# Kernel optimization log

Hardware: AMD Instinct MI355X
Metric: run time of the kernel (lower is better)

The kernel has to match this reference:

```python
import jax, jax.numpy as jnp
import numpy as np

B, S, H = 1, 2048, 2048
NH, NKV, HD = 16, 4, 128          # heads, kv heads, head_dim
RHD = 64                          # rope head dim
QC, KVC = 1536, 512               # q / kv latent dims
EPS = 1e-6
SCALE = (HD + RHD) ** -0.5


def rms_norm(x, w):
    var = jnp.mean(x.astype(jnp.float32) ** 2, axis=-1, keepdims=True)
    return (x * jax.lax.rsqrt(var + EPS) * w).astype(x.dtype)


def rotate_half(x):
    x1, x2 = x[..., : x.shape[-1] // 2], x[..., x.shape[-1] // 2:]
    return jnp.concatenate([-x2, x1], axis=-1)


def apply_rope(q, k, cos, sin):
    cos = cos[:, None, :, :]  # [B,1,S,RHD]
    sin = sin[:, None, :, :]
    return q * cos + rotate_half(q) * sin, k * cos + rotate_half(k) * sin


def setup_inputs() -> dict:
    key = jax.random.key(0)
    ks = jax.random.split(key, 12)
    X = jax.random.normal(ks[0], (B, S, H), jnp.float32)
    # rotary tables
    inv_freq = 1.0 / (10000.0 ** (np.arange(0, RHD, 2, dtype=np.float32) / RHD))
    t = np.arange(S, dtype=np.float32)
    freqs = np.outer(t, inv_freq)               # [S, RHD/2]
    emb = np.concatenate([freqs, freqs], -1)    # [S, RHD]
    cos = jnp.asarray(np.cos(emb))[None].repeat(B, 0)
    sin = jnp.asarray(np.sin(emb))[None].repeat(B, 0)
    mask = jnp.tril(jnp.ones((S, S), jnp.int32))[None].repeat(B, 0)  # causal
    sc = lambda fan_in: 1.0 / np.sqrt(fan_in)
    return dict(
        X=X, cos=cos, sin=sin, mask=mask,
        w_down_q=jax.random.normal(ks[1], (H, QC), jnp.float32) * sc(H),
        w_up_q=jax.random.normal(ks[2], (QC, H), jnp.float32) * sc(QC),
        w_qr=jax.random.normal(ks[3], (QC, NH * RHD), jnp.float32) * sc(QC),
        w_down_kv=jax.random.normal(ks[4], (H, KVC), jnp.float32) * sc(H),
        w_up_k=jax.random.normal(ks[5], (KVC, NKV * HD), jnp.float32) * sc(KVC),
        w_up_v=jax.random.normal(ks[6], (KVC, NKV * HD), jnp.float32) * sc(KVC),
        w_kr=jax.random.normal(ks[7], (H, RHD), jnp.float32) * sc(H),
        w_o=jax.random.normal(ks[8], (H, H), jnp.float32) * sc(H),
        q_norm_w=jnp.ones((QC,), jnp.float32),
        k_norm_w=jnp.ones((KVC,), jnp.float32),
    )


def reference(X, cos, sin, mask, w_down_q, w_up_q, w_qr, w_down_kv,
              w_up_k, w_up_v, w_kr, w_o, q_norm_w, k_norm_w):
    bsz, q_len, _ = X.shape
    n_rep = NH // NKV
    # --- Q path: down-project, RMSNorm, up-project + rope branch ---
    cq = rms_norm(X @ w_down_q, q_norm_w)                    # [B,S,QC]
    qc = (cq @ w_up_q).reshape(bsz, q_len, NH, HD).transpose(0, 2, 1, 3)
    qr = (cq @ w_qr).reshape(bsz, q_len, NH, RHD).transpose(0, 2, 1, 3)
    # --- KV path ---
    ckv = rms_norm(X @ w_down_kv, k_norm_w)                  # [B,S,KVC]
    kc = (ckv @ w_up_k).reshape(bsz, q_len, NKV, HD).transpose(0, 2, 1, 3)
    kr = (X @ w_kr).reshape(bsz, q_len, 1, RHD).transpose(0, 2, 1, 3)
    kc = jnp.repeat(kc, n_rep, axis=1)                       # [B,NH,S,HD]
    kr = jnp.broadcast_to(kr, (bsz, NH, q_len, RHD))         # repeat_kv(kr, NH)
    qr, kr = apply_rope(qr, kr, cos, sin)
    query = jnp.concatenate([qc, qr], axis=-1)               # [B,NH,S,HD+RHD]
    key = jnp.concatenate([kc, kr], axis=-1)
    value = (ckv @ w_up_v).reshape(bsz, q_len, NKV, HD).transpose(0, 2, 1, 3)
    value = jnp.repeat(value, n_rep, axis=1)                 # [B,NH,S,HD]
    # --- attention ---
    scores = jnp.einsum('bhqd,bhkd->bhqk', query, key) * SCALE
    scores = jnp.where(mask[:, None] == 0, -1e9, scores)
    attn = jax.nn.softmax(scores, axis=-1)                   # dropout p=0
    ctx = jnp.einsum('bhqk,bhkd->bhqd', attn, value)
    ctx = ctx.transpose(0, 2, 1, 3).reshape(bsz, q_len, NH * HD)
    return ctx @ w_o, attn
```

## Files before the change

### kernel.cpp

```cpp
#include <hip/hip_runtime.h>
#include <stdint.h>

typedef __bf16 bf16;
typedef __bf16 bf16x8 __attribute__((ext_vector_type(8)));
typedef __bf16 bf16x4 __attribute__((ext_vector_type(4)));
typedef float f32x4 __attribute__((ext_vector_type(4)));

#define DEVFN static __device__ __forceinline__

constexpr int S = 2048, Hdim = 2048, NH = 16, NKV = 4, HD = 128, RHD = 64, QC = 1536, KVC = 512;
constexpr int QKD = HD + RHD;
constexpr int DN = 2112;
constexpr float RMS_EPS = 1e-6f;
constexpr float ATT_SCALE = 0.07216878364870323f;

DEVFN float wave_sum(float v) {
#pragma unroll
  for (int o = 32; o > 0; o >>= 1) v += __shfl_xor(v, o, 64);
  return v;
}
DEVFN float block_sum(float v) {
  __shared__ float red_s[4];
  v = wave_sum(v);
  int lane = threadIdx.x & 63, wid = threadIdx.x >> 6;
  if (lane == 0) red_s[wid] = v;
  __syncthreads();
  v = red_s[0] + red_s[1] + red_s[2] + red_s[3];
  __syncthreads();
  return v;
}

DEVFN void lgkm_barrier() {
  asm volatile("s_waitcnt lgkmcnt(0)" ::: "memory");
  __builtin_amdgcn_s_barrier();
}

DEVFN void gload16(const bf16* g, bf16* l) {
  __builtin_amdgcn_global_load_lds(
      (const __attribute__((address_space(1))) uint32_t*)g,
      (__attribute__((address_space(3))) uint32_t*)l, 16, 0, 0);
}

template <typename OT>
DEVFN void gemm_core_async(const bf16* __restrict__ A, const bf16* __restrict__ Bt,
                           OT* __restrict__ C, int N, int lda, int ldb, int ldc,
                           int m0, int n0, float scale, int kend) {
  __shared__ alignas(16) bf16 As[128 * 32];
  __shared__ alignas(16) bf16 Bs[128 * 32];
  const int t = threadIdx.x;
  const int lane = t & 63;
  const int wm = ((t >> 7) & 1) * 64;
  const int wn = ((t >> 6) & 1) * 64;
  const int lr = lane & 15;
  const int lk = (lane >> 4) * 8;
  const int srow = t >> 2;
  const int scol = (t & 3) * 8;
  const bf16* Ab = A + (size_t)(m0 + srow) * lda + scol;
  const bf16* Bb = Bt + (size_t)(n0 + srow) * ldb + scol;
  bf16* Al = As + t * 8;
  bf16* Bl = Bs + t * 8;

  f32x4 acc[4][4];
#pragma unroll
  for (int i = 0; i < 4; i++)
#pragma unroll
    for (int j = 0; j < 4; j++) { f32x4 z = {0.f, 0.f, 0.f, 0.f}; acc[i][j] = z; }

  for (int kk = 0; kk < kend; kk += 32) {
    gload16(Ab + kk, Al);
    gload16(Ab + (size_t)64 * lda + kk, Al + 2048);
    gload16(Bb + kk, Bl);
    gload16(Bb + (size_t)64 * ldb + kk, Bl + 2048);
    __syncthreads();
    bf16x8 a[4], b[4];
#pragma unroll
    for (int i = 0; i < 4; i++)
      a[i] = *reinterpret_cast<const bf16x8*>(&As[(wm + i * 16 + lr) * 32 + lk]);
#pragma unroll
    for (int i = 0; i < 4; i++)
      b[i] = *reinterpret_cast<const bf16x8*>(&Bs[(wn + i * 16 + lr) * 32 + lk]);
#pragma unroll
    for (int i = 0; i < 4; i++)
#pragma unroll
      for (int j = 0; j < 4; j++)
        acc[i][j] = __builtin_amdgcn_mfma_f32_16x16x32_bf16(a[i], b[j], acc[i][j], 0, 0, 0);
    __syncthreads();
  }
  const int orow = (lane >> 4) * 4;
#pragma unroll
  for (int i = 0; i < 4; i++) {
#pragma unroll
    for (int j = 0; j < 4; j++) {
      int col = n0 + wn + j * 16 + lr;
      if (col < N) {
#pragma unroll
        for (int q = 0; q < 4; q++) {
          int row = m0 + wm + i * 16 + orow + q;
          C[(size_t)row * ldc + col] = (OT)(acc[i][j][q] * scale);
        }
      }
    }
  }
}

template <typename OT>
__global__ __launch_bounds__(256) void gemm_nt(const bf16* __restrict__ A, const bf16* __restrict__ Bt,
                                               OT* __restrict__ C, int N, int K, int lda,
                                               int ldb, int ldc, float scale) {
  gemm_core_async<OT>(A, Bt, C, N, lda, ldb, ldc, blockIdx.y * 128, blockIdx.x * 128, scale, K);
}

__global__ __launch_bounds__(256) void gemm_up_both(const bf16* __restrict__ cqb,
                                                    const bf16* __restrict__ ckvb,
                                                    const bf16* __restrict__ wt_up1,
                                                    const bf16* __restrict__ wt_up2,
                                                    bf16* __restrict__ up1,
                                                    bf16* __restrict__ up2) {
  int id = blockIdx.x;
  if (id < 384) {
    gemm_core_async<bf16>(cqb, wt_up1, up1, 3072, QC, QC, 3072, (id / 24) * 128, (id % 24) * 128, 1.f, QC);
  } else {
    id -= 384;
    gemm_core_async<bf16>(ckvb, wt_up2, up2, 1024, KVC, KVC, 1024, (id / 8) * 128, (id % 8) * 128, 1.f, KVC);
  }
}

__global__ __launch_bounds__(512) void fa_fused(const bf16* __restrict__ qpack,
                                                const bf16* __restrict__ kpack,
                                                const bf16* __restrict__ vt,
                                                float* __restrict__ attn,
                                                bf16* __restrict__ ctxb) {
  const int h = blockIdx.y;
  const int g = h >> 2;
  __shared__ alignas(16) bf16 Qs[64 * 200];
  __shared__ alignas(16) bf16 Ks[2][64 * 200];
  __shared__ alignas(16) bf16 Ps[64 * 72];
  __shared__ alignas(16) bf16 Vs[2][128 * 72];
  float2* sb = reinterpret_cast<float2*>(Ps);
  float2* statf = sb + 128;

  const int t = threadIdx.x;
  const int lane = t & 63;
  const int w = t >> 6;
  const int wm = (w & 3) * 16;
  const int kh = w >> 2;
  const int lr = lane & 15;
  const int hi = lane >> 4;
  const int lk = hi * 8;
  const int kr0 = t / 24, kc0 = (t % 24) * 8;
  const int kr1 = (t + 512) / 24, kc1 = ((t + 512) % 24) * 8;
  const int kr2 = (t + 1024) / 24, kc2 = ((t + 1024) % 24) * 8;
  const int vr0 = t >> 3, vc0 = (t & 7) * 8;
  const int vr1 = (t + 512) >> 3, vc1 = ((t + 512) & 7) * 8;

  const bf16* Qg = qpack + (size_t)h * S * QKD;
  const bf16* Kg = kpack + (size_t)g * S * QKD;
  const bf16* Vg = vt + (size_t)g * HD * S;
  float* Ah = attn + (size_t)h * S * S;
  bf16* C = ctxb + h * HD;

  for (int sub = 0; sub < 2; ++sub) {
    const int m0 = sub ? (1984 - 64 * blockIdx.x) : (64 * blockIdx.x);
    const int ntiles = sub ? (32 - blockIdx.x) : (blockIdx.x + 1);
    const int kend = m0 + 64;
    __syncthreads();
    *reinterpret_cast<bf16x8*>(&Qs[kr0 * 200 + kc0]) =
        *reinterpret_cast<const bf16x8*>(&Qg[(size_t)(m0 + kr0) * QKD + kc0]);
    *reinterpret_cast<bf16x8*>(&Qs[kr1 * 200 + kc1]) =
        *reinterpret_cast<const bf16x8*>(&Qg[(size_t)(m0 + kr1) * QKD + kc1]);
    *reinterpret_cast<bf16x8*>(&Qs[kr2 * 200 + kc2]) =
        *reinterpret_cast<const bf16x8*>(&Qg[(size_t)(m0 + kr2) * QKD + kc2]);

    float mreg[4] = {-1e30f, -1e30f, -1e30f, -1e30f};
    float lreg[4] = {0.f, 0.f, 0.f, 0.f};
    bf16x8 ck0 = *reinterpret_cast<const bf16x8*>(&Kg[(size_t)kr0 * QKD + kc0]);
    bf16x8 ck1 = *reinterpret_cast<const bf16x8*>(&Kg[(size_t)kr1 * QKD + kc1]);
    bf16x8 ck2 = *reinterpret_cast<const bf16x8*>(&Kg[(size_t)kr2 * QKD + kc2]);
    int cur = 0;
    for (int ti = 0; ti < ntiles; ++ti) {
      const int kt = ti * 64;
      bf16x8 nk0, nk1, nk2;
      if (ti + 1 < ntiles) {
        nk0 = *reinterpret_cast<const bf16x8*>(&Kg[(size_t)(kt + 64 + kr0) * QKD + kc0]);
        nk1 = *reinterpret_cast<const bf16x8*>(&Kg[(size_t)(kt + 64 + kr1) * QKD + kc1]);
        nk2 = *reinterpret_cast<const bf16x8*>(&Kg[(size_t)(kt + 64 + kr2) * QKD + kc2]);
      }
      *reinterpret_cast<bf16x8*>(&Ks[cur][kr0 * 200 + kc0]) = ck0;
      *reinterpret_cast<bf16x8*>(&Ks[cur][kr1 * 200 + kc1]) = ck1;
      *reinterpret_cast<bf16x8*>(&Ks[cur][kr2 * 200 + kc2]) = ck2;
      lgkm_barrier();
      f32x4 acc[2];
#pragma unroll
      for (int kb = 0; kb < 2; kb++) { f32x4 z = {0.f, 0.f, 0.f, 0.f}; acc[kb] = z; }
#pragma unroll
      for (int ks = 0; ks < 6; ++ks) {
        bf16x8 a = *reinterpret_cast<const bf16x8*>(&Qs[(wm + lr) * 200 + ks * 32 + lk]);
#pragma unroll
        for (int kb = 0; kb < 2; ++kb) {
          bf16x8 b = *reinterpret_cast<const bf16x8*>(&Ks[cur][(kh * 32 + kb * 16 + lr) * 200 + ks * 32 + lk]);
          acc[kb] = __builtin_amdgcn_mfma_f32_16x16x32_bf16(a, b, acc[kb], 0, 0, 0);
        }
      }
      const int colb = kt + kh * 32 + lr;
#pragma unroll
      for (int q = 0; q < 4; ++q) {
        const int rowg = m0 + wm + hi * 4 + q;
        bool u0 = (colb <= rowg), u1 = (colb + 16 <= rowg);
        float s0 = u0 ? acc[0][q] * ATT_SCALE : -1e30f;
        float s1 = u1 ? acc[1][q] * ATT_SCALE : -1e30f;
        float nm = fmaxf(mreg[q], fmaxf(s0, s1));
        float e0 = u0 ? __expf(s0 - nm) : 0.f;
        float e1 = u1 ? __expf(s1 - nm) : 0.f;
        lreg[q] = lreg[q] * __expf(mreg[q] - nm) + e0 + e1;
        mreg[q] = nm;
      }
      ck0 = nk0; ck1 = nk1; ck2 = nk2;
      cur ^= 1;
    }
#pragma unroll
    for (int q = 0; q < 4; ++q) {
      float m = mreg[q], l = lreg[q];
#pragma unroll
      for (int o = 1; o < 16; o <<= 1) {
        float mo = __shfl_xor(m, o, 64);
        float lo = __shfl_xor(l, o, 64);
        float M = fmaxf(m, mo);
        l = l * __expf(m - M) + lo * __expf(mo - M);
        m = M;
      }
      mreg[q] = m; lreg[q] = l;
    }
    __syncthreads();
    if (lr == 0) {
#pragma unroll
      for (int q = 0; q < 4; ++q)
        sb[kh * 64 + wm + hi * 4 + q] = make_float2(mreg[q], lreg[q]);
    }
    __syncthreads();
    if (w < 4 && lr == 0) {
#pragma unroll
      for (int q = 0; q < 4; ++q) {
        int r = wm + hi * 4 + q;
        float2 a = sb[r], b = sb[64 + r];
        float M = fmaxf(a.x, b.x);
        float L = a.y * __expf(a.x - M) + b.y * __expf(b.x - M);
        statf[r] = make_float2(M, 1.0f / L);
      }
    }
    __syncthreads();
    float mr[4], invl[4];
#pragma unroll
    for (int q = 0; q < 4; ++q) {
      float2 sv = statf[wm + hi * 4 + q];
      mr[q] = sv.x; invl[q] = sv.y;
    }
    __syncthreads();

    f32x4 accp[4];
#pragma unroll
    for (int j = 0; j < 4; j++) { f32x4 z = {0.f, 0.f, 0.f, 0.f}; accp[j] = z; }
    ck0 = *reinterpret_cast<const bf16x8*>(&Kg[(size_t)kr0 * QKD + kc0]);
    ck1 = *reinterpret_cast<const bf16x8*>(&Kg[(size_t)kr1 * QKD + kc1]);
    ck2 = *reinterpret_cast<const bf16x8*>(&Kg[(size_t)kr2 * QKD + kc2]);
    bf16x8 cv0 = *reinterpret_cast<const bf16x8*>(&Vg[(size_t)vr0 * S + vc0]);
    bf16x8 cv1 = *reinterpret_cast<const bf16x8*>(&Vg[(size_t)vr1 * S + vc1]);
    cur = 0;
    for (int ti = 0; ti < ntiles; ++ti) {
      const int kt = ti * 64;
      bf16x8 nk0, nk1, nk2, nv0, nv1;
      if (ti + 1 < ntiles) {
        nk0 = *reinterpret_cast<const bf16x8*>(&Kg[(size_t)(kt + 64 + kr0) * QKD + kc0]);
        nk1 = *reinterpret_cast<const bf16x8*>(&Kg[(size_t)(kt + 64 + kr1) * QKD + kc1]);
        nk2 = *reinterpret_cast<const bf16x8*>(&Kg[(size_t)(kt + 64 + kr2) * QKD + kc2]);
        nv0 = *reinterpret_cast<const bf16x8*>(&Vg[(size_t)vr0 * S + kt + 64 + vc0]);
        nv1 = *reinterpret_cast<const bf16x8*>(&Vg[(size_t)vr1 * S + kt + 64 + vc1]);
      }
      *reinterpret_cast<bf16x8*>(&Ks[cur][kr0 * 200 + kc0]) = ck0;
      *reinterpret_cast<bf16x8*>(&Ks[cur][kr1 * 200 + kc1]) = ck1;
      *reinterpret_cast<bf16x8*>(&Ks[cur][kr2 * 200 + kc2]) = ck2;
      *reinterpret_cast<bf16x8*>(&Vs[cur][vr0 * 72 + vc0]) = cv0;
      *reinterpret_cast<bf16x8*>(&Vs[cur][vr1 * 72 + vc1]) = cv1;
      lgkm_barrier();
      f32x4 acc[2];
#pragma unroll
      for (int kb = 0; kb < 2; kb++) { f32x4 z = {0.f, 0.f, 0.f, 0.f}; acc[kb] = z; }
#pragma unroll
      for (int ks = 0; ks < 6; ++ks) {
        bf16x8 a = *reinterpret_cast<const bf16x8*>(&Qs[(wm + lr) * 200 + ks * 32 + lk]);
#pragma unroll
        for (int kb = 0; kb < 2; ++kb) {
          bf16x8 b = *reinterpret_cast<const bf16x8*>(&Ks[cur][(kh * 32 + kb * 16 + lr) * 200 + ks * 32 + lk]);
          acc[kb] = __builtin_amdgcn_mfma_f32_16x16x32_bf16(a, b, acc[kb], 0, 0, 0);
        }
      }
      const int colb = kt + kh * 32 + lr;
#pragma unroll
      for (int kb = 0; kb < 2; ++kb) {
#pragma unroll
        for (int q = 0; q < 4; ++q) {
          const int rloc = wm + hi * 4 + q;
          const int rowg = m0 + rloc;
          const int col = colb + kb * 16;
          float s = acc[kb][q] * ATT_SCALE;
          float p = (col <= rowg) ? __expf(s - mr[q]) * invl[q] : 0.f;
          Ah[(size_t)rowg * S + col] = p;
          Ps[rloc * 72 + kh * 32 + kb * 16 + lr] = (bf16)p;
        }
      }
      lgkm_barrier();
#pragma unroll
      for (int ks = 0; ks < 2; ++ks) {
        bf16x8 a = *reinterpret_cast<const bf16x8*>(&Ps[(wm + lr) * 72 + ks * 32 + lk]);
#pragma unroll
        for (int j = 0; j < 4; ++j) {
          bf16x8 b = *reinterpret_cast<const bf16x8*>(&Vs[cur][(kh * 64 + j * 16 + lr) * 72 + ks * 32 + lk]);
          accp[j] = __builtin_amdgcn_mfma_f32_16x16x32_bf16(a, b, accp[j], 0, 0, 0);
        }
      }
      ck0 = nk0; ck1 = nk1; ck2 = nk2; cv0 = nv0; cv1 = nv1;
      cur ^= 1;
    }

    const float4 zz = make_float4(0.f, 0.f, 0.f, 0.f);
    {
      const int zr = t >> 3, zc0 = (t & 7) * 4;
      float* zrow = Ah + (size_t)(m0 + zr) * S;
      for (int k = kend + zc0; k < S; k += 32) *reinterpret_cast<float4*>(zrow + k) = zz;
    }

#pragma unroll
    for (int j = 0; j < 4; ++j) {
      const int d = kh * 64 + j * 16 + lr;
#pragma unroll
      for (int q = 0; q < 4; ++q) {
        const int rowg = m0 + wm + hi * 4 + q;
        C[(size_t)rowg * Hdim + d] = (bf16)accp[j][q];
      }
    }
  }
}

struct TJobs {
  const float* src[8];
  bf16* dst[8];
  int R[8], C[8], tiles[8];
};

__global__ __launch_bounds__(256) void prep(const float* __restrict__ Xf,
                                            bf16* __restrict__ Xb, TJobs J) {
  const int t = threadIdx.x;
  int id = blockIdx.x;
  if (id < 2048) {
    size_t i = (size_t)id * 256 + t;
    float4 f0 = *reinterpret_cast<const float4*>(Xf + i * 8);
    float4 f1 = *reinterpret_cast<const float4*>(Xf + i * 8 + 4);
    bf16x8 v;
    v[0] = (bf16)f0.x; v[1] = (bf16)f0.y; v[2] = (bf16)f0.z; v[3] = (bf16)f0.w;
    v[4] = (bf16)f1.x; v[5] = (bf16)f1.y; v[6] = (bf16)f1.z; v[7] = (bf16)f1.w;
    *reinterpret_cast<bf16x8*>(Xb + i * 8) = v;
    return;
  }
  int tile = id - 2048;
  int j = 0;
  while (tile >= J.tiles[j]) { tile -= J.tiles[j]; ++j; }
  const int C = J.C[j], R = J.R[j];
  int tcn = C >> 5;
  int rb = (tile / tcn) * 32, cb = (tile % tcn) * 32;
  const float* in = J.src[j];
  bf16* out = J.dst[j];
  __shared__ float tl[32][33];
  int tx = t & 31, ty = t >> 5;
#pragma unroll
  for (int q = 0; q < 32; q += 8)
    tl[ty + q][tx] = in[(size_t)(rb + ty + q) * C + cb + tx];
  __syncthreads();
#pragma unroll
  for (int q = 0; q < 32; q += 8)
    out[(size_t)(cb + ty + q) * R + rb + tx] = (bf16)tl[tx][ty + q];
}

__global__ __launch_bounds__(256) void rmsnorm_fused(const float* __restrict__ dproj,
                                                     const float* __restrict__ qw,
                                                     const float* __restrict__ kw,
                                                     bf16* __restrict__ cqb,
                                                     bf16* __restrict__ ckvb) {
  int row = blockIdx.x;
  bool isq = (blockIdx.y == 0);
  int C = isq ? QC : KVC;
  const float* p = dproj + (size_t)row * DN + (isq ? 0 : QC);
  const float* w = isq ? qw : kw;
  bf16* out = (isq ? cqb : ckvb) + (size_t)row * C;
  float ss = 0.f;
  for (int i = threadIdx.x * 4; i < C; i += 1024) {
    float4 v = *reinterpret_cast<const float4*>(p + i);
    ss += v.x * v.x + v.y * v.y + v.z * v.z + v.w * v.w;
  }
  ss = block_sum(ss);
  float r = rsqrtf(ss / (float)C + RMS_EPS);
  for (int i = threadIdx.x * 4; i < C; i += 1024) {
    float4 v = *reinterpret_cast<const float4*>(p + i);
    float4 g = *reinterpret_cast<const float4*>(w + i);
    bf16x4 o;
    o[0] = (bf16)(v.x * r * g.x); o[1] = (bf16)(v.y * r * g.y);
    o[2] = (bf16)(v.z * r * g.z); o[3] = (bf16)(v.w * r * g.w);
    *reinterpret_cast<bf16x4*>(out + i) = o;
  }
}

__global__ __launch_bounds__(256) void pack_all(const bf16* __restrict__ up1,
                                                const bf16* __restrict__ up2,
                                                const float* __restrict__ dproj,
                                                const float* __restrict__ cosp,
                                                const float* __restrict__ sinp,
                                                bf16* __restrict__ qpack,
                                                bf16* __restrict__ kpack,
                                                bf16* __restrict__ vt) {
  const int t = threadIdx.x;
  int id = blockIdx.x;
  if (id < 3072) {
    int idx = id * 256 + t;
    const int P = NH * S * 16;
    if (idx < P) {
      int d8 = idx & 15, s = (idx >> 4) & (S - 1), h = idx >> 15;
      int4 v = *reinterpret_cast<const int4*>(up1 + (size_t)s * 3072 + h * HD + d8 * 8);
      *reinterpret_cast<int4*>(qpack + ((size_t)h * S + s) * QKD + d8 * 8) = v;
    } else {
      int j = idx - P;
      int d0 = (j & 7) * 8, s = (j >> 3) & (S - 1), h = j >> 14;
      const bf16* xr = up1 + (size_t)s * 3072 + 2048 + h * RHD;
      bf16x8 xa = *reinterpret_cast<const bf16x8*>(xr + d0);
      bf16x8 xb = *reinterpret_cast<const bf16x8*>(xr + (d0 ^ 32));
      float sign = (d0 < 32) ? -1.f : 1.f;
      const float* cr = cosp + s * RHD + d0;
      const float* sr = sinp + s * RHD + d0;
      bf16x8 o;
#pragma unroll
      for (int i = 0; i < 8; i++)
        o[i] = (bf16)((float)xa[i] * cr[i] + sign * (float)xb[i] * sr[i]);
      *reinterpret_cast<bf16x8*>(qpack + ((size_t)h * S + s) * QKD + HD + d0) = o;
    }
    return;
  }
  if (id < 3648) {
    int idx = (id - 3072) * 256 + t;
    const int P = NKV * S * 16;
    if (idx < P) {
      int d8 = idx & 15, s = (idx >> 4) & (S - 1), g = idx >> 15;
      int4 v = *reinterpret_cast<const int4*>(up2 + (size_t)s * 1024 + g * HD + d8 * 8);
      *reinterpret_cast<int4*>(kpack + ((size_t)g * S + s) * QKD + d8 * 8) = v;
    } else {
      int j = idx - P;
      int d0 = (j & 7) * 8, s = j >> 3;
      const float* xr = dproj + (size_t)s * DN + 2048;
      float4 a0 = *reinterpret_cast<const float4*>(xr + d0);
      float4 a1 = *reinterpret_cast<const float4*>(xr + d0 + 4);
      float4 b0 = *reinterpret_cast<const float4*>(xr + (d0 ^ 32));
      float4 b1 = *reinterpret_cast<const float4*>(xr + (d0 ^ 32) + 4);
      float sign = (d0 < 32) ? -1.f : 1.f;
      const float* cr = cosp + s * RHD + d0;
      const float* sr = sinp + s * RHD + d0;
      float xa[8] = {a0.x, a0.y, a0.z, a0.w, a1.x, a1.y, a1.z, a1.w};
      float xb[8] = {b0.x, b0.y, b0.z, b0.w, b1.x, b1.y, b1.z, b1.w};
      bf16x8 o;
#pragma unroll
      for (int i = 0; i < 8; i++)
        o[i] = (bf16)(xa[i] * cr[i] + sign * xb[i] * sr[i]);
#pragma unroll
      for (int g = 0; g < NKV; g++)
        *reinterpret_cast<bf16x8*>(kpack + ((size_t)g * S + s) * QKD + HD + d0) = o;
    }
    return;
  }
  int tile = id - 3648;
  int cb = (tile & 15) * 32;
  int rb = (tile >> 4) * 32;
  __shared__ float tl[32][33];
  int tx = t & 31, ty = t >> 5;
  const bf16* in = up2 + 512;
#pragma unroll
  for (int q = 0; q < 32; q += 8)
    tl[ty + q][tx] = (float)in[(size_t)(rb + ty + q) * 1024 + cb + tx];
  __syncthreads();
#pragma unroll
  for (int q = 0; q < 32; q += 8)
    vt[(size_t)(cb + ty + q) * S + rb + tx] = (bf16)tl[tx][ty + q];
}

extern "C" void kernel_launch(void* const* d_in, const int* in_sizes, int n_in, void* d_out,
                              int out_size, void* d_ws, size_t ws_size, hipStream_t stream) {
  const float* Xf = (const float*)d_in[0];
  const float* cosp = (const float*)d_in[1];
  const float* sinp = (const float*)d_in[2];
  const float* w_down_q = (const float*)d_in[4];
  const float* w_up_q = (const float*)d_in[5];
  const float* w_qr = (const float*)d_in[6];
  const float* w_down_kv = (const float*)d_in[7];
  const float* w_up_k = (const float*)d_in[8];
  const float* w_up_v = (const float*)d_in[9];
  const float* w_kr = (const float*)d_in[10];
  const float* w_o = (const float*)d_in[11];
  const float* q_norm_w = (const float*)d_in[12];
  const float* k_norm_w = (const float*)d_in[13];

  float* out0 = (float*)d_out;
  float* attn = out0 + (size_t)S * Hdim;

  char* base = (char*)d_ws;
  size_t off = 0;
  auto carve = [&](size_t bytes) -> void* {
    void* p = base + off;
    off += (bytes + 255) & ~(size_t)255;
    return p;
  };
  bf16* Xb      = (bf16*)carve((size_t)S * Hdim * 2);
  bf16* wt_down = (bf16*)carve((size_t)2176 * 2048 * 2);
  bf16* wt_up1  = (bf16*)carve((size_t)3072 * QC * 2);
  bf16* wt_up2  = (bf16*)carve((size_t)1024 * KVC * 2);
  bf16* wt_o    = (bf16*)carve((size_t)Hdim * Hdim * 2);
  float* dproj  = (float*)carve((size_t)S * DN * 4);
  bf16* cqb     = (bf16*)carve((size_t)S * QC * 2);
  bf16* ckvb    = (bf16*)carve((size_t)S * KVC * 2);
  bf16* up1     = (bf16*)carve((size_t)S * 3072 * 2);
  bf16* up2     = (bf16*)carve((size_t)S * 1024 * 2);
  bf16* qpack   = (bf16*)carve((size_t)NH * S * QKD * 2);
  bf16* kpack   = (bf16*)carve((size_t)NKV * S * QKD * 2);
  bf16* vt      = (bf16*)carve((size_t)NKV * HD * S * 2);
  bf16* ctxb    = (bf16*)carve((size_t)S * Hdim * 2);
  (void)in_sizes; (void)n_in; (void)out_size; (void)ws_size;

  TJobs J;
  const float* srcs[8] = {w_down_q, w_down_kv, w_kr, w_up_q, w_qr, w_up_k, w_up_v, w_o};
  bf16* dsts[8] = {wt_down, wt_down + (size_t)QC * 2048, wt_down + (size_t)2048 * 2048,
                   wt_up1, wt_up1 + (size_t)2048 * QC, wt_up2, wt_up2 + (size_t)512 * KVC, wt_o};
  int Rs[8] = {2048, 2048, 2048, 1536, 1536, 512, 512, 2048};
  int Cs[8] = {1536, 512, 64, 2048, 1024, 512, 512, 2048};
  int total_tiles = 0;
  for (int j = 0; j < 8; j++) {
    J.src[j] = srcs[j]; J.dst[j] = dsts[j]; J.R[j] = Rs[j]; J.C[j] = Cs[j];
    J.tiles[j] = (Rs[j] / 32) * (Cs[j] / 32);
    total_tiles += J.tiles[j];
  }

  prep<<<2048 + total_tiles, 256, 0, stream>>>(Xf, Xb, J);
  gemm_nt<float><<<dim3(17, 16), 256, 0, stream>>>(Xb, wt_down, dproj, DN, Hdim, Hdim, Hdim, DN, 1.f);
  rmsnorm_fused<<<dim3(S, 2), 256, 0, stream>>>(dproj, q_norm_w, k_norm_w, cqb, ckvb);
  gemm_up_both<<<512, 256, 0, stream>>>(cqb, ckvb, wt_up1, wt_up2, up1, up2);
  pack_all<<<4672, 256, 0, stream>>>(up1, up2, dproj, cosp, sinp, qpack, kpack, vt);
  fa_fused<<<dim3(16, NH), 512, 0, stream>>>(qpack, kpack, vt, attn, ctxb);
  gemm_nt<float><<<dim3(16, 16), 256, 0, stream>>>(ctxb, wt_o, out0, Hdim, Hdim, Hdim, Hdim, Hdim, 1.f);
}
```

Baseline: 332.5 us.

## Keep Q fragments in registers and software-pipeline PV with triple-buffered P/V

Q tiles are now loaded straight from global memory into registers (six bf16x8 fragments per lane) instead of being staged in shared memory, which removes the Qs buffer and its per-tile LDS reads. The PV matmul is deferred by one iteration: P and V are triple-buffered, so the barrier between writing P and consuming it is dropped and the previous tile's PV MFMAs overlap the current tile's softmax and stores. The last tile's PV is done after the loop behind one barrier. This adds register pressure and more shared memory for V/P, and relies on the single barrier per iteration to order the buffer reuse correctly.

```diff
diff --git a/kernel.cpp b/kernel.cpp
--- a/kernel.cpp
+++ b/kernel.cpp
@@ -132,11 +132,10 @@
                                                 bf16* __restrict__ ctxb) {
   const int h = blockIdx.y;
   const int g = h >> 2;
-  __shared__ alignas(16) bf16 Qs[64 * 200];
   __shared__ alignas(16) bf16 Ks[2][64 * 200];
-  __shared__ alignas(16) bf16 Ps[64 * 72];
-  __shared__ alignas(16) bf16 Vs[2][128 * 72];
-  float2* sb = reinterpret_cast<float2*>(Ps);
+  __shared__ alignas(16) bf16 Vs[3][128 * 72];
+  __shared__ alignas(16) bf16 Ps[3][64 * 72];
+  float2* sb = reinterpret_cast<float2*>(&Vs[0][0]);
   float2* statf = sb + 128;
 
   const int t = threadIdx.x;
@@ -164,12 +163,11 @@
     const int ntiles = sub ? (32 - blockIdx.x) : (blockIdx.x + 1);
     const int kend = m0 + 64;
     __syncthreads();
-    *reinterpret_cast<bf16x8*>(&Qs[kr0 * 200 + kc0]) =
-        *reinterpret_cast<const bf16x8*>(&Qg[(size_t)(m0 + kr0) * QKD + kc0]);
-    *reinterpret_cast<bf16x8*>(&Qs[kr1 * 200 + kc1]) =
-        *reinterpret_cast<const bf16x8*>(&Qg[(size_t)(m0 + kr1) * QKD + kc1]);
-    *reinterpret_cast<bf16x8*>(&Qs[kr2 * 200 + kc2]) =
-        *reinterpret_cast<const bf16x8*>(&Qg[(size_t)(m0 + kr2) * QKD + kc2]);
+
+    bf16x8 qf[6];
+#pragma unroll
+    for (int ks = 0; ks < 6; ++ks)
+      qf[ks] = *reinterpret_cast<const bf16x8*>(&Qg[(size_t)(m0 + wm + lr) * QKD + ks * 32 + lk]);
 
     float mreg[4] = {-1e30f, -1e30f, -1e30f, -1e30f};
     float lreg[4] = {0.f, 0.f, 0.f, 0.f};
@@ -194,11 +192,10 @@
       for (int kb = 0; kb < 2; kb++) { f32x4 z = {0.f, 0.f, 0.f, 0.f}; acc[kb] = z; }
 #pragma unroll
       for (int ks = 0; ks < 6; ++ks) {
-        bf16x8 a = *reinterpret_cast<const bf16x8*>(&Qs[(wm + lr) * 200 + ks * 32 + lk]);
 #pragma unroll
         for (int kb = 0; kb < 2; ++kb) {
           bf16x8 b = *reinterpret_cast<const bf16x8*>(&Ks[cur][(kh * 32 + kb * 16 + lr) * 200 + ks * 32 + lk]);
-          acc[kb] = __builtin_amdgcn_mfma_f32_16x16x32_bf16(a, b, acc[kb], 0, 0, 0);
+          acc[kb] = __builtin_amdgcn_mfma_f32_16x16x32_bf16(qf[ks], b, acc[kb], 0, 0, 0);
         }
       }
       const int colb = kt + kh * 32 + lr;
@@ -265,6 +262,7 @@
     bf16x8 cv0 = *reinterpret_cast<const bf16x8*>(&Vg[(size_t)vr0 * S + vc0]);
     bf16x8 cv1 = *reinterpret_cast<const bf16x8*>(&Vg[(size_t)vr1 * S + vc1]);
     cur = 0;
+    int pb = 0;
     for (int ti = 0; ti < ntiles; ++ti) {
       const int kt = ti * 64;
       bf16x8 nk0, nk1, nk2, nv0, nv1;
@@ -278,19 +276,18 @@
       *reinterpret_cast<bf16x8*>(&Ks[cur][kr0 * 200 + kc0]) = ck0;
       *reinterpret_cast<bf16x8*>(&Ks[cur][kr1 * 200 + kc1]) = ck1;
       *reinterpret_cast<bf16x8*>(&Ks[cur][kr2 * 200 + kc2]) = ck2;
-      *reinterpret_cast<bf16x8*>(&Vs[cur][vr0 * 72 + vc0]) = cv0;
-      *reinterpret_cast<bf16x8*>(&Vs[cur][vr1 * 72 + vc1]) = cv1;
+      *reinterpret_cast<bf16x8*>(&Vs[pb][vr0 * 72 + vc0]) = cv0;
+      *reinterpret_cast<bf16x8*>(&Vs[pb][vr1 * 72 + vc1]) = cv1;
       lgkm_barrier();
       f32x4 acc[2];
 #pragma unroll
       for (int kb = 0; kb < 2; kb++) { f32x4 z = {0.f, 0.f, 0.f, 0.f}; acc[kb] = z; }
 #pragma unroll
       for (int ks = 0; ks < 6; ++ks) {
-        bf16x8 a = *reinterpret_cast<const bf16x8*>(&Qs[(wm + lr) * 200 + ks * 32 + lk]);
 #pragma unroll
         for (int kb = 0; kb < 2; ++kb) {
           bf16x8 b = *reinterpret_cast<const bf16x8*>(&Ks[cur][(kh * 32 + kb * 16 + lr) * 200 + ks * 32 + lk]);
-          acc[kb] = __builtin_amdgcn_mfma_f32_16x16x32_bf16(a, b, acc[kb], 0, 0, 0);
+          acc[kb] = __builtin_amdgcn_mfma_f32_16x16x32_bf16(qf[ks], b, acc[kb], 0, 0, 0);
         }
       }
       const int colb = kt + kh * 32 + lr;
@@ -304,21 +301,37 @@
           float s = acc[kb][q] * ATT_SCALE;
           float p = (col <= rowg) ? __expf(s - mr[q]) * invl[q] : 0.f;
           Ah[(size_t)rowg * S + col] = p;
-          Ps[rloc * 72 + kh * 32 + kb * 16 + lr] = (bf16)p;
+          Ps[pb][rloc * 72 + kh * 32 + kb * 16 + lr] = (bf16)p;
         }
       }
-      lgkm_barrier();
+      if (ti > 0) {
+        const int pp = (pb == 0) ? 2 : pb - 1;
+#pragma unroll
+        for (int ks = 0; ks < 2; ++ks) {
+          bf16x8 a = *reinterpret_cast<const bf16x8*>(&Ps[pp][(wm + lr) * 72 + ks * 32 + lk]);
+#pragma unroll
+          for (int j = 0; j < 4; ++j) {
+            bf16x8 b = *reinterpret_cast<const bf16x8*>(&Vs[pp][(kh * 64 + j * 16 + lr) * 72 + ks * 32 + lk]);
+            accp[j] = __builtin_amdgcn_mfma_f32_16x16x32_bf16(a, b, accp[j], 0, 0, 0);
+          }
+        }
+      }
+      ck0 = nk0; ck1 = nk1; ck2 = nk2; cv0 = nv0; cv1 = nv1;
+      cur ^= 1;
+      pb = (pb == 2) ? 0 : pb + 1;
+    }
+    lgkm_barrier();
+    {
+      const int pp = (pb == 0) ? 2 : pb - 1;
 #pragma unroll
       for (int ks = 0; ks < 2; ++ks) {
-        bf16x8 a = *reinterpret_cast<const bf16x8*>(&Ps[(wm + lr) * 72 + ks * 32 + lk]);
+        bf16x8 a = *reinterpret_cast<const bf16x8*>(&Ps[pp][(wm + lr) * 72 + ks * 32 + lk]);
 #pragma unroll
         for (int j = 0; j < 4; ++j) {
-          bf16x8 b = *reinterpret_cast<const bf16x8*>(&Vs[cur][(kh * 64 + j * 16 + lr) * 72 + ks * 32 + lk]);
+          bf16x8 b = *reinterpret_cast<const bf16x8*>(&Vs[pp][(kh * 64 + j * 16 + lr) * 72 + ks * 32 + lk]);
           accp[j] = __builtin_amdgcn_mfma_f32_16x16x32_bf16(a, b, accp[j], 0, 0, 0);
         }
       }
-      ck0 = nk0; ck1 = nk1; ck2 = nk2; cv0 = nv0; cv1 = nv1;
-      cur ^= 1;
     }
 
     const float4 zz = make_float4(0.f, 0.f, 0.f, 0.f);
```

Measured after the change: 310.0 us. -6.8%, faster.
